# Kernel tuning notes

Hardware: AMD Instinct MI355X
Metric: run time of the kernel (lower is better)

## Reference

```python
import jax, jax.numpy as jnp
import numpy as np

D_MODEL = 1024
NUM_HEADS = 16
HEAD_DIM = D_MODEL // NUM_HEADS
ROT_DIM = 32
THETA = 10000.0
XPOS_SCALE_BASE = 512.0
GN_EPS = 1e-5


def setup_inputs() -> dict:
    key = jax.random.key(0)
    ks = jax.random.split(key, 12)
    d = D_MODEL
    s = 0.02
    return {
        "x": jax.random.normal(ks[0], (2, 2048, d), dtype=jnp.float32),
        "Wq": jax.random.normal(ks[1], (d, d), dtype=jnp.float32) * s,
        "bq": jnp.zeros((d,), jnp.float32),
        "Wk": jax.random.normal(ks[2], (d, d), dtype=jnp.float32) * s,
        "bk": jnp.zeros((d,), jnp.float32),
        "Wv": jax.random.normal(ks[3], (d, d), dtype=jnp.float32) * s,
        "bv": jnp.zeros((d,), jnp.float32),
        "Wg": jax.random.normal(ks[4], (d, d), dtype=jnp.float32) * s,
        "bg": jnp.zeros((d,), jnp.float32),
        "Wo": jax.random.normal(ks[5], (d, d), dtype=jnp.float32) * s,
        "bo": jnp.zeros((d,), jnp.float32),
        "gn_w": jnp.ones((NUM_HEADS,), jnp.float32),
        "gn_b": jnp.zeros((NUM_HEADS,), jnp.float32),
    }


def _rotate_half(x):
    # interleaved pair rotation: (x1, x2) -> (-x2, x1)
    x1 = x[..., 0::2]
    x2 = x[..., 1::2]
    return jnp.stack([-x2, x1], axis=-1).reshape(x.shape)


def _rotary_xpos(q, k):
    # q, k: [B, H, S, HEAD_DIM]; rotate first ROT_DIM dims with xpos scaling
    S = q.shape[-2]
    inv_freq = 1.0 / (THETA ** (jnp.arange(0, ROT_DIM, 2, dtype=jnp.float32) / ROT_DIM))
    t = jnp.arange(S, dtype=jnp.float32)
    freqs = jnp.repeat(t[:, None] * inv_freq[None, :], 2, axis=-1)  # [S, ROT_DIM]
    base = (jnp.arange(0, ROT_DIM, 2, dtype=jnp.float32) + 0.4 * ROT_DIM) / (1.4 * ROT_DIM)
    power = (t - S // 2) / XPOS_SCALE_BASE
    scale = jnp.repeat(base[None, :] ** power[:, None], 2, axis=-1)  # [S, ROT_DIM]
    cos, sin = jnp.cos(freqs), jnp.sin(freqs)

    def apply(x, s):
        xm, xr = x[..., :ROT_DIM], x[..., ROT_DIM:]
        xm = xm * (cos * s) + _rotate_half(xm) * (sin * s)
        return jnp.concatenate([xm, xr], axis=-1)

    return apply(q, scale), apply(k, 1.0 / scale)


def _decay_mask(S):
    # per-head causal decay mask, row-normalized by sqrt(row sum)
    h = jnp.arange(NUM_HEADS, dtype=jnp.float32)
    gamma = 1.0 - 2.0 ** (-5.0 - h)                       # [H]
    idx = jnp.arange(S)
    pw = (idx[:, None] - idx[None, :]).astype(jnp.float32)  # [S, S]
    mask = jnp.where(pw >= 0, gamma[:, None, None] ** pw, 0.0)  # [H, S, S]
    return mask / jnp.sqrt(jnp.sum(mask, axis=-1, keepdims=True))


def _heads(x):
    B, S, _ = x.shape
    return x.reshape(B, S, NUM_HEADS, HEAD_DIM).transpose(0, 2, 1, 3)


def reference(x, Wq, bq, Wk, bk, Wv, bv, Wg, bg, Wo, bo, gn_w, gn_b):
    B, S, d = x.shape
    q = _heads(x @ Wq + bq)
    k = _heads(x @ Wk + bk)
    v = _heads(x @ Wv + bv)
    q, k = _rotary_xpos(q, k)

    mask = _decay_mask(S)                                  # [H, S, S]
    scores = jnp.einsum("bhqd,bhkd->bhqk", q, k) * mask[None]
    ret = jnp.einsum("bhqk,bhkd->bhqd", scores, v)         # [B, H, S, HEAD_DIM]

    # GroupNorm(num_groups=H, num_channels=H): normalize each head over (S, D)
    mean = jnp.mean(ret, axis=(2, 3), keepdims=True)
    var = jnp.var(ret, axis=(2, 3), keepdims=True)
    ret = (ret - mean) / jnp.sqrt(var + GN_EPS)
    ret = ret * gn_w[None, :, None, None] + gn_b[None, :, None, None]

    concat = ret.transpose(0, 2, 1, 3).reshape(B, S, d)
    gate = jax.nn.silu(x @ Wg + bg)
    return (gate * concat) @ Wo + bo
```

## Files before the change

### kernel.cpp

```cpp
#include <hip/hip_runtime.h>
#include <math.h>

constexpr int B = 2;
constexpr int S = 2048;
constexpr int DMODEL = 1024;
constexpr int H = 16;
constexpr int M_TOT = B * S;
constexpr size_t MAT = (size_t)B * S * DMODEL;

typedef __attribute__((ext_vector_type(8))) __bf16 bf16x8;
typedef __attribute__((ext_vector_type(4))) float f32x4;

#define GLOAD16(g, l) __builtin_amdgcn_global_load_lds( \
    (const __attribute__((address_space(1))) void*)(g), \
    (__attribute__((address_space(3))) void*)(l), 16, 0, 0)

__device__ __forceinline__ float bf2f(__bf16 v) { return (float)v; }
__device__ __forceinline__ __bf16 f2bf(float v) { return (__bf16)v; }
__device__ __forceinline__ float silu(float z) { return z / (1.0f + expf(-z)); }

__global__ __launch_bounds__(256) void prep_kernel(
    const float* __restrict__ x, __bf16* __restrict__ xb,
    const float* Wq, const float* Wk, const float* Wv, const float* Wg,
    const float* Wo, __bf16* __restrict__ wqkvg_t, __bf16* __restrict__ wo_t,
    const float* bq, const float* bk, const float* bv, const float* bg,
    float* __restrict__ bqkvg)
{
    __shared__ float tile[32][33];
    const int bid = blockIdx.x;
    const int tid = threadIdx.x;

    if (bid < 2048) {
        const size_t p = (size_t)bid * 256 + tid;
        const float4 a = reinterpret_cast<const float4*>(x)[2 * p];
        const float4 b = reinterpret_cast<const float4*>(x)[2 * p + 1];
        bf16x8 o;
        o[0] = f2bf(a.x); o[1] = f2bf(a.y); o[2] = f2bf(a.z); o[3] = f2bf(a.w);
        o[4] = f2bf(b.x); o[5] = f2bf(b.y); o[6] = f2bf(b.z); o[7] = f2bf(b.w);
        reinterpret_cast<bf16x8*>(xb)[p] = o;
    } else if (bid < 7168) {
        const int idx = bid - 2048;
        const int z = idx >> 10;
        const int rem = idx & 1023;
        const int n0 = (rem & 31) * 32, k0 = (rem >> 5) * 32;
        const float* W = (z == 0) ? Wq : (z == 1) ? Wk : (z == 2) ? Wv
                        : (z == 3) ? Wg : Wo;
        const int tx = tid & 31, ty = tid >> 5;
        #pragma unroll
        for (int i = 0; i < 32; i += 8)
            tile[ty + i][tx] = W[(size_t)(k0 + ty + i) * DMODEL + n0 + tx];
        __syncthreads();
        #pragma unroll
        for (int i = 0; i < 32; i += 8) {
            const int n = n0 + ty + i, kk = k0 + tx;
            const __bf16 val = f2bf(tile[tx][ty + i]);
            if (z < 4) wqkvg_t[((size_t)z * 1024 + n) * DMODEL + kk] = val;
            else       wo_t[(size_t)n * DMODEL + kk] = val;
        }
    } else {
        const int i = (bid - 7168) * 256 + tid;
        const float* src = ((i >> 10) == 0) ? bq : ((i >> 10) == 1) ? bk
                          : ((i >> 10) == 2) ? bv : bg;
        bqkvg[i] = src[i & 1023];
    }
}

__device__ __forceinline__ bf16x8 ldsfrag(const char* base, int row, int kbyte)
{
    return *(const bf16x8*)(base + row * 64 + (kbyte ^ (((row >> 1) & 3) << 4)));
}

__global__ __launch_bounds__(512, 4) void gemm_qkvg(
    const __bf16* __restrict__ A, const __bf16* __restrict__ Bt,
    const float* __restrict__ bias,
    __bf16* o0, __bf16* o1, __bf16* o2, __bf16* o3)
{
    __shared__ char lds[49152];
    constexpr int NTK = 32;

    const int tid = threadIdx.x, wv = tid >> 6, ln = tid & 63;
    const int wm = wv >> 1, wn = wv & 1;

    int bid = blockIdx.x;
    bid = (bid & 7) * 64 + (bid >> 3);
    const int bx = bid & 31, by = bid >> 5;
    const int row0 = by * 256, col0 = bx * 128;

    const int lrow = ln & 15;
    const int kb   = (ln >> 4) * 16;

    f32x4 acc[4][4] = {};

    auto stageA = [&](int k0, char* buf) {
        #pragma unroll
        for (int j = 0; j < 2; ++j) {
            const int r  = j * 128 + (tid >> 2);
            const int cb = ((tid & 3) * 16) ^ (((r >> 1) & 3) << 4);
            GLOAD16((const char*)(A + ((size_t)(row0 + r) << 10) + k0) + cb,
                    buf + j * 8192 + wv * 1024);
        }
    };
    auto stageB = [&](int k0, char* buf) {
        const int r  = tid >> 2;
        const int cb = ((tid & 3) * 16) ^ (((r >> 1) & 3) << 4);
        GLOAD16((const char*)(Bt + ((size_t)(col0 + r) << 10) + k0) + cb,
                buf + wv * 1024);
    };

    stageA(0, lds);
    stageB(0, lds + 32768);

    for (int t = 0; t < NTK; ++t) {
        char* ab = lds + (t & 1) * 16384;
        char* bb = lds + 32768 + (t & 1) * 8192;

        if (t + 1 < NTK) {
            stageA((t + 1) * 32, lds + ((t + 1) & 1) * 16384);
            stageB((t + 1) * 32, lds + 32768 + ((t + 1) & 1) * 8192);
            asm volatile("s_waitcnt vmcnt(3)" ::: "memory");
        } else {
            asm volatile("s_waitcnt vmcnt(0)" ::: "memory");
        }
        __builtin_amdgcn_s_barrier();
        __builtin_amdgcn_sched_barrier(0);

        bf16x8 af[4], bf[4];
        #pragma unroll
        for (int mf = 0; mf < 4; ++mf)
            af[mf] = ldsfrag(ab, wm * 64 + mf * 16 + lrow, kb);
        #pragma unroll
        for (int nf = 0; nf < 4; ++nf)
            bf[nf] = ldsfrag(bb, wn * 64 + nf * 16 + lrow, kb);

        __builtin_amdgcn_s_setprio(1);
        #pragma unroll
        for (int mf = 0; mf < 4; ++mf)
            #pragma unroll
            for (int nf = 0; nf < 4; ++nf)
                acc[mf][nf] = __builtin_amdgcn_mfma_f32_16x16x32_bf16(
                    af[mf], bf[nf], acc[mf][nf], 0, 0, 0);
        __builtin_amdgcn_s_setprio(0);

        __builtin_amdgcn_s_barrier();
        __builtin_amdgcn_sched_barrier(0);
    }

    const int sel = col0 >> 10;
    __bf16* outp = (sel == 0) ? o0 : (sel == 1) ? o1 : (sel == 2) ? o2 : o3;
    const int cb0 = col0 & 1023;

    if (sel <= 1) {
        const bool isQ = (sel == 0);
        #pragma unroll
        for (int nf = 0; nf < 4; ++nf) {
            const int cl = cb0 + wn * 64 + nf * 16 + (ln & 15);
            const int h = cl >> 6, d0 = cl & 63;
            const float bs = bias[col0 + wn * 64 + nf * 16 + (ln & 15)];
            const float l2g = log2f(1.0f - exp2f(-5.0f - (float)h));
            const bool rot = (d0 < 32);
            float invf = 0.0f, l2base = 0.0f;
            if (rot) {
                const int j = d0 >> 1;
                invf = powf(10000.0f, -(float)j / 16.0f);
                l2base = log2f((2.0f * j + 12.8f) / 44.8f);
                if (!isQ) l2base = -l2base;
            }
            const bool isEven = ((d0 & 1) == 0);
            #pragma unroll
            for (int mf = 0; mf < 4; ++mf) {
                #pragma unroll
                for (int reg = 0; reg < 4; ++reg) {
                    const int r = row0 + wm * 64 + mf * 16 + (ln >> 4) * 4 + reg;
                    const int s = r & (S - 1);
                    const int sloc = s & 63;
                    float v = acc[mf][nf][reg] + bs;
                    const float wdec = isQ
                        ? exp2f((float)(sloc + 1) * l2g)
                        : exp2f((float)(63 - sloc) * l2g);
                    if (rot) {
                        const float freq = (float)s * invf;
                        const float c = cosf(freq), sn = sinf(freq);
                        const float pexp = ((float)s - 1024.0f) * (1.0f / 512.0f);
                        const float sc = exp2f(l2base * pexp);
                        const float partner = __shfl_xor(v, 1, 64);
                        v = isEven ? (v * c - partner * sn)
                                   : (v * c + partner * sn);
                        v *= sc;
                    }
                    outp[(size_t)r * 1024 + cl] = f2bf(v * wdec);
                }
            }
        }
    } else {
        #pragma unroll
        for (int mf = 0; mf < 4; ++mf) {
            #pragma unroll
            for (int nf = 0; nf < 4; ++nf) {
                const int cl = cb0 + wn * 64 + nf * 16 + (ln & 15);
                const float bs = bias[col0 + wn * 64 + nf * 16 + (ln & 15)];
                #pragma unroll
                for (int reg = 0; reg < 4; ++reg) {
                    const int r = row0 + wm * 64 + mf * 16 + (ln >> 4) * 4 + reg;
                    outp[(size_t)r * 1024 + cl] = f2bf(acc[mf][nf][reg] + bs);
                }
            }
        }
    }
}

__global__ __launch_bounds__(256) void gemm_wo_kernel(
    const __bf16* __restrict__ A, const __bf16* __restrict__ Bt,
    const float* __restrict__ bias, float* __restrict__ fout)
{
    __shared__ char lds[49152];
    constexpr int NTK = 32;

    const int tid = threadIdx.x, wv = tid >> 6, ln = tid & 63;
    const int row0 = blockIdx.y * 128, col0 = blockIdx.x * 64;
    const int wr = (wv >> 1) * 64, wc = (wv & 1) * 32;
    const int lrow = ln & 15, kb = (ln >> 4) * 16;

    f32x4 acc[4][2] = {};

    auto stageA = [&](int k0, char* buf) {
        #pragma unroll
        for (int j = 0; j < 2; ++j) {
            const int r  = j * 64 + (tid >> 2);
            const int cb = ((tid & 3) * 16) ^ (((r >> 1) & 3) << 4);
            GLOAD16((const char*)(A + ((size_t)(row0 + r) << 10) + k0) + cb,
                    buf + j * 4096 + wv * 1024);
        }
    };
    auto stageB = [&](int k0, char* buf) {
        const int r  = tid >> 2;
        const int cb = ((tid & 3) * 16) ^ (((r >> 1) & 3) << 4);
        GLOAD16((const char*)(Bt + ((size_t)(col0 + r) << 10) + k0) + cb,
                buf + wv * 1024);
    };

    #pragma unroll
    for (int tt = 0; tt < 3; ++tt) {
        stageA(tt * 32, lds + tt * 8192);
        stageB(tt * 32, lds + 32768 + tt * 4096);
    }
    asm volatile("s_waitcnt vmcnt(6)" ::: "memory");
    __builtin_amdgcn_s_barrier();
    __builtin_amdgcn_sched_barrier(0);

    for (int t = 0; t < NTK; ++t) {
        const char* ab = lds + (t & 3) * 8192;
        const char* bb = lds + 32768 + (t & 3) * 4096;
        bf16x8 af[4], bf[2];
        #pragma unroll
        for (int mi = 0; mi < 4; ++mi)
            af[mi] = ldsfrag(ab, wr + mi * 16 + lrow, kb);
        #pragma unroll
        for (int ni = 0; ni < 2; ++ni)
            bf[ni] = ldsfrag(bb, wc + ni * 16 + lrow, kb);

        if (t + 3 < NTK) {
            stageA((t + 3) * 32, lds + ((t + 3) & 3) * 8192);
            stageB((t + 3) * 32, lds + 32768 + ((t + 3) & 3) * 4096);
        }

        __builtin_amdgcn_s_setprio(1);
        #pragma unroll
        for (int mi = 0; mi < 4; ++mi)
            #pragma unroll
            for (int ni = 0; ni < 2; ++ni)
                acc[mi][ni] = __builtin_amdgcn_mfma_f32_16x16x32_bf16(
                    af[mi], bf[ni], acc[mi][ni], 0, 0, 0);
        __builtin_amdgcn_s_setprio(0);

        if (t <= NTK - 4)
            asm volatile("s_waitcnt vmcnt(6)" ::: "memory");
        else if (t == NTK - 3)
            asm volatile("s_waitcnt vmcnt(3)" ::: "memory");
        else if (t == NTK - 2)
            asm volatile("s_waitcnt vmcnt(0)" ::: "memory");
        __builtin_amdgcn_s_barrier();
        __builtin_amdgcn_sched_barrier(0);
    }

    #pragma unroll
    for (int mi = 0; mi < 4; ++mi) {
        #pragma unroll
        for (int ni = 0; ni < 2; ++ni) {
            const int c = col0 + wc + ni * 16 + (ln & 15);
            const float bs = bias[c];
            #pragma unroll
            for (int reg = 0; reg < 4; ++reg) {
                const int r = row0 + wr + mi * 16 + (ln >> 4) * 4 + reg;
                fout[(size_t)r * DMODEL + c] = acc[mi][ni][reg] + bs;
            }
        }
    }
}

__global__ __launch_bounds__(256) void chunk_prep_kernel(
    const __bf16* __restrict__ kg, const __bf16* __restrict__ vg,
    __bf16* __restrict__ vt, float* __restrict__ U)
{
    __shared__ __bf16 ktile[64][72];
    __shared__ __bf16 vtile[64][72];
    __shared__ __bf16 ktl[64 * 64];
    __shared__ __bf16 vtl[64 * 64];

    const int c = blockIdx.x, h = blockIdx.y, b = blockIdx.z;
    const int bh = b * 16 + h;
    const int t = threadIdx.x, wv = t >> 6, ln = t & 63;
    const int lrow = ln & 15, lk8 = (ln >> 4) * 8;
    const size_t rowbase = ((size_t)b * S + c * 64) * DMODEL + h * 64;

    #pragma unroll
    for (int p = 0; p < 2; ++p) {
        const int ci = p * 256 + t;
        const int r = ci >> 3, c8 = (ci & 7) * 8;
        *reinterpret_cast<bf16x8*>(&ktile[r][c8]) =
            *reinterpret_cast<const bf16x8*>(&kg[rowbase + (size_t)r * DMODEL + c8]);
        *reinterpret_cast<bf16x8*>(&vtile[r][c8]) =
            *reinterpret_cast<const bf16x8*>(&vg[rowbase + (size_t)r * DMODEL + c8]);
    }
    __syncthreads();

    #pragma unroll
    for (int p = 0; p < 2; ++p) {
        const int ci = p * 256 + t;
        const int d = ci >> 3, s8 = (ci & 7) * 8;
        bf16x8 ok, ov;
        #pragma unroll
        for (int w = 0; w < 8; ++w) {
            ok[w] = ktile[s8 + w][d];
            ov[w] = vtile[s8 + w][d];
        }
        *reinterpret_cast<bf16x8*>(
            &vt[((size_t)bh * 64 + d) * 2048 + c * 64 + s8]) = ov;
        const int off = d * 128 + ((s8 * 2) ^ ((d & 7) << 4));
        *(bf16x8*)((char*)ktl + off) = ok;
        *(bf16x8*)((char*)vtl + off) = ov;
    }
    __syncthreads();

    f32x4 uacc[4] = {};
    #pragma unroll
    for (int ks = 0; ks < 2; ++ks) {
        const int arow = wv * 16 + lrow;
        const bf16x8 af = *(const bf16x8*)((char*)vtl + arow * 128 +
            (((ks * 32 + lk8) * 2) ^ ((arow & 7) << 4)));
        #pragma unroll
        for (int nf = 0; nf < 4; ++nf) {
            const int brow = nf * 16 + lrow;
            const bf16x8 bf_ = *(const bf16x8*)((char*)ktl + brow * 128 +
                (((ks * 32 + lk8) * 2) ^ ((brow & 7) << 4)));
            uacc[nf] = __builtin_amdgcn_mfma_f32_16x16x32_bf16(
                af, bf_, uacc[nf], 0, 0, 0);
        }
    }

    const size_t ub = ((size_t)bh * 32 + c) * 4096;
    #pragma unroll
    for (int nf = 0; nf < 4; ++nf) {
        const int dk = nf * 16 + (ln & 15);
        #pragma unroll
        for (int reg = 0; reg < 4; ++reg) {
            const int dv = wv * 16 + (ln >> 4) * 4 + reg;
            U[ub + dv * 64 + dk] = uacc[nf][reg];
        }
    }
}

__global__ __launch_bounds__(256) void chunk_scan_kernel(
    const float* __restrict__ U, __bf16* __restrict__ St)
{
    const int dvq = blockIdx.x, bh = blockIdx.y;
    const int h = bh & 15;
    const float gamma = 1.0f - exp2f(-5.0f - (float)h);
    const float g64 = exp2f(64.0f * log2f(gamma));
    const int t = threadIdx.x;
    const int dk = t & 63;
    const int dv0 = dvq * 16 + (t >> 6) * 4;
    float s0 = 0.f, s1 = 0.f, s2 = 0.f, s3 = 0.f;
    const size_t ub = (size_t)bh * 32 * 4096;
    for (int c = 0; c < 32; ++c) {
        const size_t sb = ub + (size_t)c * 4096;
        St[sb + (dv0 + 0) * 64 + dk] = f2bf(s0);
        St[sb + (dv0 + 1) * 64 + dk] = f2bf(s1);
        St[sb + (dv0 + 2) * 64 + dk] = f2bf(s2);
        St[sb + (dv0 + 3) * 64 + dk] = f2bf(s3);
        s0 = g64 * s0 + U[sb + (dv0 + 0) * 64 + dk];
        s1 = g64 * s1 + U[sb + (dv0 + 1) * 64 + dk];
        s2 = g64 * s2 + U[sb + (dv0 + 2) * 64 + dk];
        s3 = g64 * s3 + U[sb + (dv0 + 3) * 64 + dk];
    }
}

__global__ __launch_bounds__(256) void retention_chunk_kernel(
    const __bf16* __restrict__ qg, const __bf16* __restrict__ kg,
    const __bf16* __restrict__ vt, const __bf16* __restrict__ St,
    __bf16* __restrict__ retb, float* __restrict__ part)
{
    __shared__ __bf16 qh[64 * 64];
    __shared__ __bf16 kh[64 * 64];
    __shared__ __bf16 vl[64 * 64];
    __shared__ __bf16 sl[64 * 64];
    __shared__ __bf16 pl[64 * 64];
    __shared__ float rs[4], rq[4];

    const int c = blockIdx.x, h = blockIdx.y, b = blockIdx.z;
    const int bh = b * 16 + h;
    const int t = threadIdx.x, wv = t >> 6, ln = t & 63;
    const int lrow = ln & 15, lk8 = (ln >> 4) * 8;

    const float gamma = 1.0f - exp2f(-5.0f - (float)h);
    const float l2g   = log2f(gamma);
    const float gm64i = exp2f(-64.0f * l2g);
    const size_t rowbase = ((size_t)b * S + c * 64) * DMODEL + h * 64;
    const size_t vtb = (size_t)bh * 64 * 2048 + c * 64;
    const size_t stb = ((size_t)bh * 32 + c) * 4096;

    #pragma unroll
    for (int p = 0; p < 2; ++p) {
        const int ci = p * 256 + t;
        const int r = ci >> 3, c8 = (ci & 7) * 8;
        const int off = r * 128 + ((c8 * 2) ^ ((r & 7) << 4));
        *(bf16x8*)((char*)qh + off) =
            *reinterpret_cast<const bf16x8*>(&qg[rowbase + (size_t)r * DMODEL + c8]);
        *(bf16x8*)((char*)kh + off) =
            *reinterpret_cast<const bf16x8*>(&kg[rowbase + (size_t)r * DMODEL + c8]);
        *(bf16x8*)((char*)vl + off) =
            *reinterpret_cast<const bf16x8*>(&vt[vtb + (size_t)r * 2048 + c8]);
        *(bf16x8*)((char*)sl + off) =
            *reinterpret_cast<const bf16x8*>(&St[stb + r * 64 + c8]);
    }
    __syncthreads();

    f32x4 sacc[4] = {};
    #pragma unroll
    for (int ks = 0; ks < 2; ++ks) {
        const int qrow = wv * 16 + lrow;
        const bf16x8 qf = *(const bf16x8*)((char*)qh + qrow * 128 +
            (((ks * 32 + lk8) * 2) ^ ((qrow & 7) << 4)));
        #pragma unroll
        for (int mi = 0; mi < 4; ++mi) {
            const int krow = mi * 16 + lrow;
            const bf16x8 kf = *(const bf16x8*)((char*)kh + krow * 128 +
                (((ks * 32 + lk8) * 2) ^ ((krow & 7) << 4)));
            sacc[mi] = __builtin_amdgcn_mfma_f32_16x16x32_bf16(
                kf, qf, sacc[mi], 0, 0, 0);
        }
    }

    const int iw = wv * 16 + (ln & 15);
    #pragma unroll
    for (int mi = 0; mi < 4; ++mi) {
        ushort4 pk;
        unsigned short* pkp = (unsigned short*)&pk;
        #pragma unroll
        for (int reg = 0; reg < 4; ++reg) {
            const int j = mi * 16 + (ln >> 4) * 4 + reg;
            const float pv = (j <= iw) ? sacc[mi][reg] * gm64i : 0.0f;
            const __bf16 pb = f2bf(pv);
            pkp[reg] = *(const unsigned short*)&pb;
        }
        const int jb8 = mi * 16 + (ln >> 4) * 4;
        *(ushort4*)((char*)pl + iw * 128 + ((jb8 * 2) ^ ((iw & 7) << 4))) = pk;
    }

    f32x4 acc[4] = {};
    #pragma unroll
    for (int ks = 0; ks < 2; ++ks) {
        const int prow = wv * 16 + lrow;
        const bf16x8 pf = *(const bf16x8*)((char*)pl + prow * 128 +
            (((ks * 32 + lk8) * 2) ^ ((prow & 7) << 4)));
        const bf16x8 qf2 = *(const bf16x8*)((char*)qh + prow * 128 +
            (((ks * 32 + lk8) * 2) ^ ((prow & 7) << 4)));
        #pragma unroll
        for (int nd = 0; nd < 4; ++nd) {
            const int vrow = nd * 16 + lrow;
            const bf16x8 vf = *(const bf16x8*)((char*)vl + vrow * 128 +
                (((ks * 32 + lk8) * 2) ^ ((vrow & 7) << 4)));
            const bf16x8 sf = *(const bf16x8*)((char*)sl + vrow * 128 +
                (((ks * 32 + lk8) * 2) ^ ((vrow & 7) << 4)));
            acc[nd] = __builtin_amdgcn_mfma_f32_16x16x32_bf16(
                pf, vf, acc[nd], 0, 0, 0);
            acc[nd] = __builtin_amdgcn_mfma_f32_16x16x32_bf16(
                qf2, sf, acc[nd], 0, 0, 0);
        }
    }

    const float sc5h = exp2f(5.0f + (float)h);
    float psum = 0.0f, psq = 0.0f;
    #pragma unroll
    for (int reg = 0; reg < 4; ++reg) {
        const int i = c * 64 + wv * 16 + (ln >> 4) * 4 + reg;
        const float omg = 1.0f - exp2f((float)(i + 1) * l2g);
        const float invn = rsqrtf(omg * sc5h);
        #pragma unroll
        for (int nd = 0; nd < 4; ++nd) {
            const float v = acc[nd][reg] * invn;
            retb[((size_t)b * S + i) * DMODEL + h * 64 + nd * 16 + (ln & 15)] =
                f2bf(v);
            psum += v;
            psq  += v * v;
        }
    }
    #pragma unroll
    for (int o = 32; o > 0; o >>= 1) {
        psum += __shfl_down(psum, o, 64);
        psq  += __shfl_down(psq, o, 64);
    }
    if (ln == 0) { rs[wv] = psum; rq[wv] = psq; }
    __syncthreads();
    if (t == 0) {
        part[((size_t)bh * 32 + c) * 2 + 0] = rs[0] + rs[1] + rs[2] + rs[3];
        part[((size_t)bh * 32 + c) * 2 + 1] = rq[0] + rq[1] + rq[2] + rq[3];
    }
}

__global__ __launch_bounds__(64) void gn_stats2_kernel(const float* __restrict__ part,
                                                       float* __restrict__ stats)
{
    const int bh = threadIdx.x;
    if (bh < 32) {
        float s = 0.0f, q2 = 0.0f;
        for (int i = 0; i < 32; ++i) {
            s  += part[(bh * 32 + i) * 2 + 0];
            q2 += part[(bh * 32 + i) * 2 + 1];
        }
        const float inv_n = 1.0f / (float)(S * 64);
        const float mean = s * inv_n;
        const float var  = q2 * inv_n - mean * mean;
        stats[bh * 2 + 0] = mean;
        stats[bh * 2 + 1] = rsqrtf(var + 1e-5f);
    }
}

__global__ __launch_bounds__(256) void gn_apply_kernel(
    const __bf16* __restrict__ retb, const __bf16* __restrict__ g,
    __bf16* __restrict__ y, const float* __restrict__ stats,
    const float* __restrict__ gnw, const float* __restrict__ gnb)
{
    const size_t p = (size_t)blockIdx.x * 256 + threadIdx.x;
    const size_t el = p * 8;
    const int col = (int)(el & (DMODEL - 1));
    const int h   = col >> 6;
    const int b   = (int)(el >> 21);
    const int bh  = b * H + h;
    const float mean = stats[bh * 2 + 0];
    const float w    = stats[bh * 2 + 1] * gnw[h];
    const float bb   = gnb[h];

    const bf16x8 rv = reinterpret_cast<const bf16x8*>(retb)[p];
    const bf16x8 gv = reinterpret_cast<const bf16x8*>(g)[p];
    bf16x8 o;
    #pragma unroll
    for (int i = 0; i < 8; ++i)
        o[i] = f2bf(((bf2f(rv[i]) - mean) * w + bb) * silu(bf2f(gv[i])));
    reinterpret_cast<bf16x8*>(y)[p] = o;
}

extern "C" void kernel_launch(void* const* d_in, const int* in_sizes, int n_in,
                              void* d_out, int out_size, void* d_ws, size_t ws_size,
                              hipStream_t stream)
{
    const float* x   = (const float*)d_in[0];
    const float* Wq  = (const float*)d_in[1];
    const float* bq  = (const float*)d_in[2];
    const float* Wk  = (const float*)d_in[3];
    const float* bk  = (const float*)d_in[4];
    const float* Wv  = (const float*)d_in[5];
    const float* bv  = (const float*)d_in[6];
    const float* Wg  = (const float*)d_in[7];
    const float* bg  = (const float*)d_in[8];
    const float* Wo  = (const float*)d_in[9];
    const float* bo  = (const float*)d_in[10];
    const float* gnw = (const float*)d_in[11];
    const float* gnb = (const float*)d_in[12];
    float* out = (float*)d_out;

    char* w = (char*)d_ws;
    __bf16* xb      = (__bf16*)w;               w += MAT * 2;
    __bf16* wqkvg_t = (__bf16*)w;               w += MAT * 2;
    __bf16* wo_t    = (__bf16*)w;               w += (size_t)DMODEL * DMODEL * 2;
    float*  bqkvg   = (float*)w;                w += 4096 * 4;
    __bf16* qb      = (__bf16*)w;               w += MAT * 2;
    __bf16* kb      = (__bf16*)w;               w += MAT * 2;
    __bf16* vb      = (__bf16*)w;               w += MAT * 2;
    __bf16* gb      = (__bf16*)w;               w += MAT * 2;
    __bf16* retb    = (__bf16*)w;               w += MAT * 2;
    __bf16* yb      = (__bf16*)w;               w += MAT * 2;
    float*  U       = (float*)w;                w += MAT * 4;
    float*  part    = (float*)w;                w += 2048 * 4;
    float*  stats   = (float*)w;                w += 64 * 4;
    __bf16* vt = xb;
    __bf16* St = (__bf16*)wqkvg_t;

    prep_kernel<<<7184, 256, 0, stream>>>(x, xb, Wq, Wk, Wv, Wg, Wo,
                                          wqkvg_t, wo_t, bq, bk, bv, bg, bqkvg);

    gemm_qkvg<<<512, 512, 0, stream>>>(xb, wqkvg_t, bqkvg, qb, kb, vb, gb);

    {
        dim3 grid(32, 16, 2);
        chunk_prep_kernel<<<grid, 256, 0, stream>>>(kb, vb, vt, U);
    }
    {
        dim3 grid(4, 32);
        chunk_scan_kernel<<<grid, 256, 0, stream>>>(U, St);
    }
    {
        dim3 grid(32, 16, 2);
        retention_chunk_kernel<<<grid, 256, 0, stream>>>(qb, kb, vt, St,
                                                         retb, part);
    }

    gn_stats2_kernel<<<1, 64, 0, stream>>>(part, stats);
    gn_apply_kernel<<<2048, 256, 0, stream>>>(retb, gb, yb, stats, gnw, gnb);

    {
        dim3 grid(16, 32);
        gemm_wo_kernel<<<grid, 256, 0, stream>>>(yb, wo_t, bo, out);
    }
}
```

Before: 120.0 us.

## Move rotary xpos and decay scaling out of QKVG GEMM epilogue into separate kernel

```diff
diff --git a/kernel.cpp b/kernel.cpp
--- a/kernel.cpp
+++ b/kernel.cpp
@@ -148,64 +148,70 @@
     const int sel = col0 >> 10;
     __bf16* outp = (sel == 0) ? o0 : (sel == 1) ? o1 : (sel == 2) ? o2 : o3;
     const int cb0 = col0 & 1023;
-
-    if (sel <= 1) {
-        const bool isQ = (sel == 0);
+    #pragma unroll
+    for (int mf = 0; mf < 4; ++mf) {
         #pragma unroll
         for (int nf = 0; nf < 4; ++nf) {
             const int cl = cb0 + wn * 64 + nf * 16 + (ln & 15);
-            const int h = cl >> 6, d0 = cl & 63;
             const float bs = bias[col0 + wn * 64 + nf * 16 + (ln & 15)];
-            const float l2g = log2f(1.0f - exp2f(-5.0f - (float)h));
-            const bool rot = (d0 < 32);
-            float invf = 0.0f, l2base = 0.0f;
-            if (rot) {
-                const int j = d0 >> 1;
-                invf = powf(10000.0f, -(float)j / 16.0f);
-                l2base = log2f((2.0f * j + 12.8f) / 44.8f);
-                if (!isQ) l2base = -l2base;
+            #pragma unroll
+            for (int reg = 0; reg < 4; ++reg) {
+                const int r = row0 + wm * 64 + mf * 16 + (ln >> 4) * 4 + reg;
+                outp[(size_t)r * 1024 + cl] = f2bf(acc[mf][nf][reg] + bs);
             }
-            const bool isEven = ((d0 & 1) == 0);
-            #pragma unroll
-            for (int mf = 0; mf < 4; ++mf) {
-                #pragma unroll
-                for (int reg = 0; reg < 4; ++reg) {
-                    const int r = row0 + wm * 64 + mf * 16 + (ln >> 4) * 4 + reg;
-                    const int s = r & (S - 1);
-                    const int sloc = s & 63;
-                    float v = acc[mf][nf][reg] + bs;
-                    const float wdec = isQ
-                        ? exp2f((float)(sloc + 1) * l2g)
-                        : exp2f((float)(63 - sloc) * l2g);
-                    if (rot) {
-                        const float freq = (float)s * invf;
-                        const float c = cosf(freq), sn = sinf(freq);
-                        const float pexp = ((float)s - 1024.0f) * (1.0f / 512.0f);
-                        const float sc = exp2f(l2base * pexp);
-                        const float partner = __shfl_xor(v, 1, 64);
-                        v = isEven ? (v * c - partner * sn)
-                                   : (v * c + partner * sn);
-                        v *= sc;
-                    }
-                    outp[(size_t)r * 1024 + cl] = f2bf(v * wdec);
-                }
-            }
+        }
+    }
+}
+
+__global__ __launch_bounds__(256) void rotary_bf16_kernel(__bf16* __restrict__ q,
+                                                          __bf16* __restrict__ k)
+{
+    const size_t p = (size_t)blockIdx.x * 256 + threadIdx.x;
+    const size_t el = p * 8;
+    const int bs = (int)(el >> 10);
+    const int col = (int)(el & 1023);
+    const int h = col >> 6, d0 = col & 63;
+    const int s = bs & (S - 1);
+    const int sloc = s & 63;
+
+    const float gamma = 1.0f - exp2f(-5.0f - (float)h);
+    const float l2g   = log2f(gamma);
+    const float wq = exp2f((float)(sloc + 1) * l2g);
+    const float wk = exp2f((float)(63 - sloc) * l2g);
+
+    bf16x8 qv = reinterpret_cast<const bf16x8*>(q)[p];
+    bf16x8 kv = reinterpret_cast<const bf16x8*>(k)[p];
+    bf16x8 qo, ko;
+
+    if (d0 < 32) {
+        const float pexp = ((float)s - (float)(S / 2)) / 512.0f;
+        #pragma unroll
+        for (int w = 0; w < 4; ++w) {
+            const int j = (d0 >> 1) + w;
+            const float inv_freq = powf(10000.0f, -(float)j / 16.0f);
+            const float freq = (float)s * inv_freq;
+            const float c  = cosf(freq);
+            const float sn = sinf(freq);
+            const float base = (2.0f * j + 0.4f * 32.0f) / (1.4f * 32.0f);
+            const float sc   = powf(base, pexp);
+
+            const float q0 = bf2f(qv[2 * w]), q1 = bf2f(qv[2 * w + 1]);
+            qo[2 * w]     = f2bf((q0 * c - q1 * sn) * sc * wq);
+            qo[2 * w + 1] = f2bf((q1 * c + q0 * sn) * sc * wq);
+            const float isc = 1.0f / sc;
+            const float k0 = bf2f(kv[2 * w]), k1 = bf2f(kv[2 * w + 1]);
+            ko[2 * w]     = f2bf((k0 * c - k1 * sn) * isc * wk);
+            ko[2 * w + 1] = f2bf((k1 * c + k0 * sn) * isc * wk);
         }
     } else {
         #pragma unroll
-        for (int mf = 0; mf < 4; ++mf) {
-            #pragma unroll
-            for (int nf = 0; nf < 4; ++nf) {
-                const int cl = cb0 + wn * 64 + nf * 16 + (ln & 15);
-                const float bs = bias[col0 + wn * 64 + nf * 16 + (ln & 15)];
-                #pragma unroll
-                for (int reg = 0; reg < 4; ++reg) {
-                    const int r = row0 + wm * 64 + mf * 16 + (ln >> 4) * 4 + reg;
-                    outp[(size_t)r * 1024 + cl] = f2bf(acc[mf][nf][reg] + bs);
-                }
-            }
-        }
-    }
+        for (int w = 0; w < 8; ++w) {
+            qo[w] = f2bf(bf2f(qv[w]) * wq);
+            ko[w] = f2bf(bf2f(kv[w]) * wk);
+        }
+    }
+    reinterpret_cast<bf16x8*>(q)[p] = qo;
+    reinterpret_cast<bf16x8*>(k)[p] = ko;
 }
 
 __global__ __launch_bounds__(256) void gemm_wo_kernel(
@@ -600,6 +606,8 @@
 
     gemm_qkvg<<<512, 512, 0, stream>>>(xb, wqkvg_t, bqkvg, qb, kb, vb, gb);
 
+    rotary_bf16_kernel<<<2048, 256, 0, stream>>>(qb, kb);
+
     {
         dim3 grid(32, 16, 2);
         chunk_prep_kernel<<<grid, 256, 0, stream>>>(kb, vb, vt, U);
```

Result: slower. 125.8 us (+4.9%).
